# Optimization experiments

Hardware: AMD Instinct MI355X
Metric: run time of the kernel (lower is better)

## Reference

```python
import jax, jax.numpy as jnp
import numpy as np

B, D, H, E, O = 524288, 32, 64, 8, 1
H2 = H // 2


def setup_inputs() -> dict:
    key = jax.random.key(0)
    ks = jax.random.split(key, 6)
    x = jax.random.normal(ks[0], (B, D), dtype=jnp.float32)
    soft_cluster_probs = jax.random.uniform(ks[1], (B, E), dtype=jnp.float32)
    # Stacked per-expert MLP params (Dense default glorot-like scale approximated by scaled normal)
    W1 = jax.random.normal(ks[2], (E, D, H), dtype=jnp.float32) * (1.0 / np.sqrt(D))
    b1 = jnp.zeros((E, H), dtype=jnp.float32)
    W2 = jax.random.normal(ks[3], (E, H, H2), dtype=jnp.float32) * (1.0 / np.sqrt(H))
    b2 = jnp.zeros((E, H2), dtype=jnp.float32)
    W3 = jax.random.normal(ks[4], (E, H2, O), dtype=jnp.float32) * (1.0 / np.sqrt(H2))
    b3 = jnp.zeros((E, O), dtype=jnp.float32)
    return {"x": x, "soft_cluster_probs": soft_cluster_probs,
            "W1": W1, "b1": b1, "W2": W2, "b2": b2, "W3": W3, "b3": b3}


def reference(x, soft_cluster_probs, W1, b1, W2, b2, W3, b3):
    # Soft-clustering inference path: every expert processes all rows,
    # outputs combined with per-row expert weights. Dropout inactive.
    h1 = jax.nn.relu(jnp.einsum('bd,edh->ebh', x, W1) + b1[:, None, :])      # [E,B,H]
    h2 = jax.nn.relu(jnp.einsum('ebh,ehk->ebk', h1, W2) + b2[:, None, :])    # [E,B,H/2]
    eo = jax.nn.sigmoid(jnp.einsum('ebk,eko->ebo', h2, W3) + b3[:, None, :])  # [E,B,O]
    # combined = sum_e eo[e] * clustering[:, e:e+1]
    out = jnp.einsum('ebo,be->bo', eo, soft_cluster_probs)                    # [B,O]
    return out
```

## Files before the change

kernel.cpp:

```cpp
#include <hip/hip_runtime.h>


typedef __attribute__((ext_vector_type(8))) _Float16 f16x8;
typedef __attribute__((ext_vector_type(2))) __fp16 h16x2;
typedef __attribute__((ext_vector_type(4))) float f32x4;

__device__ __forceinline__ unsigned pkh(float lo, float hi) {
    union { h16x2 v; unsigned u; } t;
    t.v = __builtin_amdgcn_cvt_pkrtz(lo, hi);
    return t.u;
}

__device__ __forceinline__ unsigned relu2(unsigned a) {
    unsigned r;
    asm("v_pk_max_f16 %0, %1, 0" : "=v"(r) : "v"(a));
    return r;
}

__device__ __forceinline__ float sigf(float s) {
    return 1.f / (1.f + __expf(-s));
}

#define MFMA32(a, b, c) __builtin_amdgcn_mfma_f32_16x16x32_f16((a), (b), (c), 0, 0, 0)

__global__ __launch_bounds__(1024)
void build_image(const float* __restrict__ W1, const float* __restrict__ b1,
                 const float* __restrict__ W2, const float* __restrict__ b2,
                 const float* __restrict__ W3, const float* __restrict__ b3,
                 char* __restrict__ ws) {
    const int tid = threadIdx.x;
    #pragma unroll
    for (int k = 0; k < 4; ++k) {
        const int F = tid + k * 1024;
        const int e = (F >> 8) & 7, s = F & 255;
        const int qq = (s >> 4) & 3, nn = s & 15;
        const float* src;
        int stride;
        if (F < 2048) {
            const int mt = s >> 6;
            const int h = 32 * (mt >> 1) + 8 * (nn >> 2) + 4 * (mt & 1) + (nn & 3);
            src = W1 + (e * 32 + 8 * qq) * 64 + h;
            stride = 64;
        } else {
            const int kb2 = (s >> 7) & 1, mt2 = (s >> 6) & 1;
            const int h2 = 8 * (nn >> 2) + 4 * mt2 + (nn & 3);
            src = W2 + (e * 64 + 32 * kb2 + 8 * qq) * 32 + h2;
            stride = 32;
        }
        union { f16x8 v; unsigned u[4]; } t;
        t.u[0] = pkh(src[0 * stride], src[1 * stride]);
        t.u[1] = pkh(src[2 * stride], src[3 * stride]);
        t.u[2] = pkh(src[4 * stride], src[5 * stride]);
        t.u[3] = pkh(src[6 * stride], src[7 * stride]);
        *(f16x8*)(ws + F * 16) = t.v;
    }
    if (tid < 128) {
        const int e = tid >> 4, mt = (tid >> 2) & 3, q = tid & 3;
        *(f32x4*)(ws + 65536 + tid * 16) =
            *(const f32x4*)(b1 + e * 64 + 32 * (mt >> 1) + 4 * (mt & 1) + 8 * q);
    } else if (tid < 192) {
        const int i = tid - 128, e = i >> 3, mt2 = (i >> 2) & 1, q = i & 3;
        *(f32x4*)(ws + 67584 + i * 16) =
            *(const f32x4*)(b2 + e * 32 + 4 * mt2 + 8 * q);
    } else if (tid < 224) {
        const int i = tid - 192, e = i >> 2, q = i & 3;
        const f32x4 lo = *(const f32x4*)(W3 + e * 32 + 8 * q);
        const f32x4 hi = *(const f32x4*)(W3 + e * 32 + 8 * q + 4);
        union { f16x8 v; unsigned u[4]; } a;
        a.u[0] = pkh(lo.x, lo.y); a.u[1] = pkh(lo.z, lo.w);
        a.u[2] = pkh(hi.x, hi.y); a.u[3] = pkh(hi.z, hi.w);
        *(f16x8*)(ws + 68608 + i * 16) = a.v;
    } else if (tid < 232) {
        const int i = tid - 224;
        *(float*)(ws + 69120 + i * 4) = b3[i];
    }
}

__global__ __launch_bounds__(512, 4)
void moe_fused(const float* __restrict__ x, const float* __restrict__ probs,
               const char* __restrict__ img, float* __restrict__ out) {
    __shared__ __attribute__((aligned(16))) char ldsraw[65536];
    const int tid = threadIdx.x;
    const int w = tid >> 6, lane = tid & 63, n = lane & 15, q = lane >> 4;

    #pragma unroll
    for (int k = 0; k < 8; ++k) {
        const int off = tid * 16 + k * 8192;
        *(f32x4*)(ldsraw + off) = *(const f32x4*)(img + off);
    }

    const int rb = blockIdx.x * 512 + w * 64;
    union { f16x8 v; unsigned u[4]; } xf[4];
    #pragma unroll
    for (int rt = 0; rt < 4; ++rt) {
        const float* xp = x + (size_t)(rb + rt * 16 + n) * 32 + q * 8;
        const f32x4 xa = *(const f32x4*)xp, xb = *(const f32x4*)(xp + 4);
        xf[rt].u[0] = pkh(xa.x, xa.y); xf[rt].u[1] = pkh(xa.z, xa.w);
        xf[rt].u[2] = pkh(xb.x, xb.y); xf[rt].u[3] = pkh(xb.z, xb.w);
    }

    __syncthreads();

    const short* wl = (const short*)ldsraw + (n * 8 + q * 128);
    const char* gb1 = img + 65536 + q * 16;
    const char* gb2 = img + 67584 + q * 16;
    const char* ga3 = img + 68608 + q * 16;
    const float* gb3 = (const float*)(img + 69120);
    const float* pba = probs + (size_t)(rb + n) * 8;
    float r[4] = {0.f, 0.f, 0.f, 0.f};

    #pragma unroll 1
    for (int e = 0; e < 8; ++e) {
        const short* we = wl + e * 2048;

        union { f16x8 v; unsigned u[4]; } P[4][2];
        #pragma unroll
        for (int mt = 0; mt < 4; ++mt) {
            const f16x8 w1f = *(const f16x8*)(we + mt * 512);
            const f32x4 bf = *(const f32x4*)(gb1 + e * 256 + mt * 64);
            f32x4 c[4];
            #pragma unroll
            for (int rt = 0; rt < 4; ++rt) c[rt] = MFMA32(w1f, xf[rt].v, bf);
            #pragma unroll
            for (int rt = 0; rt < 4; ++rt) {
                P[rt][mt >> 1].u[(mt & 1) * 2 + 0] = relu2(pkh(c[rt].x, c[rt].y));
                P[rt][mt >> 1].u[(mt & 1) * 2 + 1] = relu2(pkh(c[rt].z, c[rt].w));
            }
        }

        union { f16x8 v; unsigned u[4]; } PC[4];
        #pragma unroll
        for (int mt2 = 0; mt2 < 2; ++mt2) {
            const f32x4 bf = *(const f32x4*)(gb2 + e * 128 + mt2 * 64);
            f32x4 c[4];
            #pragma unroll
            for (int rt = 0; rt < 4; ++rt) c[rt] = bf;
            #pragma unroll
            for (int kb2 = 0; kb2 < 2; ++kb2) {
                const f16x8 w2f =
                    *(const f16x8*)(we + 16384 + mt2 * 512 + kb2 * 1024);
                #pragma unroll
                for (int rt = 0; rt < 4; ++rt)
                    c[rt] = MFMA32(w2f, P[rt][kb2].v, c[rt]);
            }
            #pragma unroll
            for (int rt = 0; rt < 4; ++rt) {
                PC[rt].u[mt2 * 2 + 0] = relu2(pkh(c[rt].x, c[rt].y));
                PC[rt].u[mt2 * 2 + 1] = relu2(pkh(c[rt].z, c[rt].w));
            }
        }

        const f16x8 a3v = *(const f16x8*)(ga3 + e * 64);
        const float bb = gb3[e];
        const f32x4 cb = {bb, bb, bb, bb};
        #pragma unroll
        for (int rt = 0; rt < 4; ++rt) {
            const f32x4 s = MFMA32(a3v, PC[rt].v, cb);
            r[rt] = fmaf(sigf(s.x), pba[e + rt * 128], r[rt]);
        }
    }

    if (q == 0) {
        #pragma unroll
        for (int rt = 0; rt < 4; ++rt) out[rb + rt * 16 + n] = r[rt];
    }
}

extern "C" void kernel_launch(void* const* d_in, const int* in_sizes, int n_in,
                              void* d_out, int out_size, void* d_ws, size_t ws_size,
                              hipStream_t stream) {
    const float* x     = (const float*)d_in[0];
    const float* probs = (const float*)d_in[1];
    const float* W1    = (const float*)d_in[2];
    const float* b1    = (const float*)d_in[3];
    const float* W2    = (const float*)d_in[4];
    const float* b2    = (const float*)d_in[5];
    const float* W3    = (const float*)d_in[6];
    const float* b3    = (const float*)d_in[7];

    hipLaunchKernelGGL(build_image, dim3(1), dim3(1024), 0, stream,
                       W1, b1, W2, b2, W3, b3, (char*)d_ws);
    const int nrows = in_sizes[0] / 32;
    hipLaunchKernelGGL(moe_fused, dim3(nrows / 512), dim3(512), 0, stream,
                       x, probs, (const char*)d_ws, (float*)d_out);
}
```

Baseline: 156.2 us.

## Assign one expert per wave with weights held in registers

Each of the 8 waves in a block now owns one expert and keeps that expert's W1/W2/W3 fragments in registers. All waves sweep the same 512 rows in chunks of 64. Per-expert gated outputs are written to a double-buffered LDS area, and wave 0 sums them after a block barrier. This removes the 64KB LDS weight image and the per-expert LDS weight reads, which allows higher occupancy. In exchange it adds a __syncthreads per 64-row chunk, each wave re-reads the same x rows (8x redundant loads served from cache), and the final reduction is serialized onto one wave.

```diff
diff --git a/kernel.cpp b/kernel.cpp
--- a/kernel.cpp
+++ b/kernel.cpp
@@ -4,6 +4,7 @@
 typedef __attribute__((ext_vector_type(8))) _Float16 f16x8;
 typedef __attribute__((ext_vector_type(2))) __fp16 h16x2;
 typedef __attribute__((ext_vector_type(4))) float f32x4;
+typedef union { f16x8 v; unsigned u[4]; } Fu;
 
 __device__ __forceinline__ unsigned pkh(float lo, float hi) {
     union { h16x2 v; unsigned u; } t;
@@ -79,48 +80,60 @@
 __global__ __launch_bounds__(512, 4)
 void moe_fused(const float* __restrict__ x, const float* __restrict__ probs,
                const char* __restrict__ img, float* __restrict__ out) {
-    __shared__ __attribute__((aligned(16))) char ldsraw[65536];
+    __shared__ __attribute__((aligned(16))) char lds[8192];
     const int tid = threadIdx.x;
     const int w = tid >> 6, lane = tid & 63, n = lane & 15, q = lane >> 4;
-
+    const int e = w;
+
+    if (tid < 226) {
+        *(f32x4*)(lds + 4096 + tid * 16) = *(const f32x4*)(img + 65536 + tid * 16);
+    }
+
+    const int lo = n * 16 + q * 256;
+    Fu w1r[4], w2r[2][2], a3r;
     #pragma unroll
-    for (int k = 0; k < 8; ++k) {
-        const int off = tid * 16 + k * 8192;
-        *(f32x4*)(ldsraw + off) = *(const f32x4*)(img + off);
-    }
-
-    const int rb = blockIdx.x * 512 + w * 64;
-    union { f16x8 v; unsigned u[4]; } xf[4];
+    for (int mt = 0; mt < 4; ++mt)
+        w1r[mt].v = *(const f16x8*)(img + e * 4096 + mt * 1024 + lo);
     #pragma unroll
-    for (int rt = 0; rt < 4; ++rt) {
-        const float* xp = x + (size_t)(rb + rt * 16 + n) * 32 + q * 8;
-        const f32x4 xa = *(const f32x4*)xp, xb = *(const f32x4*)(xp + 4);
-        xf[rt].u[0] = pkh(xa.x, xa.y); xf[rt].u[1] = pkh(xa.z, xa.w);
-        xf[rt].u[2] = pkh(xb.x, xb.y); xf[rt].u[3] = pkh(xb.z, xb.w);
-    }
-
+    for (int mt2 = 0; mt2 < 2; ++mt2)
+        #pragma unroll
+        for (int kb2 = 0; kb2 < 2; ++kb2)
+            w2r[mt2][kb2].v =
+                *(const f16x8*)(img + 32768 + e * 4096 + kb2 * 2048 + mt2 * 1024 + lo);
+    a3r.v = *(const f16x8*)(img + 68608 + e * 64 + q * 16);
+    const float b3v = *(const float*)(img + 69120 + e * 4);
+
+    const char* bb1 = lds + 4096 + e * 256 + q * 16;
+    const char* bb2 = lds + 6144 + e * 128 + q * 16;
+
+    const int base = blockIdx.x * 512;
     __syncthreads();
 
-    const short* wl = (const short*)ldsraw + (n * 8 + q * 128);
-    const char* gb1 = img + 65536 + q * 16;
-    const char* gb2 = img + 67584 + q * 16;
-    const char* ga3 = img + 68608 + q * 16;
-    const float* gb3 = (const float*)(img + 69120);
-    const float* pba = probs + (size_t)(rb + n) * 8;
-    float r[4] = {0.f, 0.f, 0.f, 0.f};
-
     #pragma unroll 1
-    for (int e = 0; e < 8; ++e) {
-        const short* we = wl + e * 2048;
-
-        union { f16x8 v; unsigned u[4]; } P[4][2];
+    for (int it = 0; it < 8; ++it) {
+        const int rb = base + it * 64;
+        char* pb = lds + (it & 1) * 2048;
+
+        Fu xf[4];
+        #pragma unroll
+        for (int rt = 0; rt < 4; ++rt) {
+            const float* xp = x + (size_t)(rb + rt * 16 + n) * 32 + q * 8;
+            const f32x4 xa = *(const f32x4*)xp, xb = *(const f32x4*)(xp + 4);
+            xf[rt].u[0] = pkh(xa.x, xa.y); xf[rt].u[1] = pkh(xa.z, xa.w);
+            xf[rt].u[2] = pkh(xb.x, xb.y); xf[rt].u[3] = pkh(xb.z, xb.w);
+        }
+        float p[4];
+        #pragma unroll
+        for (int rt = 0; rt < 4; ++rt)
+            p[rt] = probs[(size_t)(rb + rt * 16 + n) * 8 + e];
+
+        Fu P[4][2];
         #pragma unroll
         for (int mt = 0; mt < 4; ++mt) {
-            const f16x8 w1f = *(const f16x8*)(we + mt * 512);
-            const f32x4 bf = *(const f32x4*)(gb1 + e * 256 + mt * 64);
+            const f32x4 bf = *(const f32x4*)(bb1 + mt * 64);
             f32x4 c[4];
             #pragma unroll
-            for (int rt = 0; rt < 4; ++rt) c[rt] = MFMA32(w1f, xf[rt].v, bf);
+            for (int rt = 0; rt < 4; ++rt) c[rt] = MFMA32(w1r[mt].v, xf[rt].v, bf);
             #pragma unroll
             for (int rt = 0; rt < 4; ++rt) {
                 P[rt][mt >> 1].u[(mt & 1) * 2 + 0] = relu2(pkh(c[rt].x, c[rt].y));
@@ -128,21 +141,18 @@
             }
         }
 
-        union { f16x8 v; unsigned u[4]; } PC[4];
+        Fu PC[4];
         #pragma unroll
         for (int mt2 = 0; mt2 < 2; ++mt2) {
-            const f32x4 bf = *(const f32x4*)(gb2 + e * 128 + mt2 * 64);
+            const f32x4 bf = *(const f32x4*)(bb2 + mt2 * 64);
             f32x4 c[4];
             #pragma unroll
             for (int rt = 0; rt < 4; ++rt) c[rt] = bf;
             #pragma unroll
-            for (int kb2 = 0; kb2 < 2; ++kb2) {
-                const f16x8 w2f =
-                    *(const f16x8*)(we + 16384 + mt2 * 512 + kb2 * 1024);
+            for (int kb2 = 0; kb2 < 2; ++kb2)
                 #pragma unroll
                 for (int rt = 0; rt < 4; ++rt)
-                    c[rt] = MFMA32(w2f, P[rt][kb2].v, c[rt]);
-            }
+                    c[rt] = MFMA32(w2r[mt2][kb2].v, P[rt][kb2].v, c[rt]);
             #pragma unroll
             for (int rt = 0; rt < 4; ++rt) {
                 PC[rt].u[mt2 * 2 + 0] = relu2(pkh(c[rt].x, c[rt].y));
@@ -150,19 +160,24 @@
             }
         }
 
-        const f16x8 a3v = *(const f16x8*)(ga3 + e * 64);
-        const float bb = gb3[e];
-        const f32x4 cb = {bb, bb, bb, bb};
+        const f32x4 cb = {b3v, b3v, b3v, b3v};
         #pragma unroll
         for (int rt = 0; rt < 4; ++rt) {
-            const f32x4 s = MFMA32(a3v, PC[rt].v, cb);
-            r[rt] = fmaf(sigf(s.x), pba[e + rt * 128], r[rt]);
-        }
-    }
-
-    if (q == 0) {
-        #pragma unroll
-        for (int rt = 0; rt < 4; ++rt) out[rb + rt * 16 + n] = r[rt];
+            const f32x4 s = MFMA32(a3r.v, PC[rt].v, cb);
+            const float g = sigf(s.x) * p[rt];
+            if (q == 0)
+                *(float*)(pb + (e * 64 + rt * 16 + n) * 4) = g;
+        }
+
+        __syncthreads();
+
+        if (w == 0) {
+            float s = 0.f;
+            #pragma unroll
+            for (int ee = 0; ee < 8; ++ee)
+                s += *(const float*)(pb + (ee * 64 + lane) * 4);
+            out[rb + lane] = s;
+        }
     }
 }
 
```

Result: slower. 186.8 us (+19.6%).
